# Kernel tuning notes

Hardware: AMD Instinct MI355X
Metric: run time of the kernel (lower is better)

The kernel has to match this reference:

```python
import jax, jax.numpy as jnp
import numpy as np
import math

B, L, D, H = 2, 2048, 1024, 16
DH = D // H  # d_head = 64
FACTOR = 5


def setup_inputs() -> dict:
    key = jax.random.key(0)
    ks = jax.random.split(key, 6)
    s = 0.02
    x = jax.random.normal(ks[0], (B, L, D), jnp.float32)
    Wq = jax.random.normal(ks[1], (D, D), jnp.float32) * s
    bq = jnp.zeros((D,), jnp.float32)
    Wkv = jax.random.normal(ks[2], (2 * D, D), jnp.float32) * s
    bkv = jnp.zeros((2 * D,), jnp.float32)
    Wout = jax.random.normal(ks[3], (D, D), jnp.float32) * s
    bout = jnp.zeros((D,), jnp.float32)
    U = min(FACTOR * math.ceil(math.log(L)), L)  # 40
    index_sample = jax.random.randint(ks[4], (L, U), 0, L, dtype=jnp.int32)
    return {"x": x, "Wq": Wq, "bq": bq, "Wkv": Wkv, "bkv": bkv,
            "Wout": Wout, "bout": bout, "index_sample": index_sample,
            "factor": FACTOR}


def reference(x, Wq, bq, Wkv, bkv, Wout, bout, index_sample, factor):
    b, l, d = x.shape
    h, dh = H, DH
    scale = 1.0 / math.sqrt(dh)
    u = min(factor * math.ceil(math.log(l)), l)

    # projections (torch Linear: y = x @ W.T + b)
    Q = (x @ Wq.T + bq).reshape(b, l, h, dh).transpose(0, 2, 1, 3)   # [B,H,L,dh]
    KV = x @ Wkv.T + bkv
    K, V = jnp.split(KV, 2, axis=-1)
    K = K.reshape(b, l, h, dh).transpose(0, 2, 1, 3)                  # [B,H,L,dh]
    V = V.reshape(b, l, h, dh).transpose(0, 2, 1, 3)                  # [B,H,L,dh]

    # sampled QK: per query position l, dot with U sampled keys
    K_s = K[:, :, index_sample, :]                                    # [B,H,L,U,dh]
    QK = jnp.einsum('bhld,bhlud->bhlu', Q, K_s)                       # [B,H,L,U]
    M = QK.max(axis=-1) - QK.mean(axis=-1)                            # sparsity measure
    _, top_idx = jax.lax.top_k(M, u)                                  # [B,H,u]

    # full attention only for the top-u queries
    top_q = jnp.take_along_axis(Q, top_idx[..., None], axis=2)        # [B,H,u,dh]
    scores = jnp.einsum('bhud,bhkd->bhuk', top_q, K) * scale          # [B,H,u,L]
    attn = jax.nn.softmax(scores, axis=-1)
    ctx_update = jnp.einsum('bhuk,bhkd->bhud', attn, V)               # [B,H,u,dh]

    # mean-initialized context, scatter updates at top queries
    context = jnp.broadcast_to(V.mean(axis=2, keepdims=True), (b, h, l, dh))
    bI = jnp.arange(b)[:, None, None]
    hI = jnp.arange(h)[None, :, None]
    context = context.at[bI, hI, top_idx].set(ctx_update)             # [B,H,L,dh]

    context = context.transpose(0, 2, 1, 3).reshape(b, l, d)
    return context @ Wout.T + bout
```

## Files before the change

### kernel.cpp

```cpp
#include <hip/hip_runtime.h>
#include <math.h>

#define B_ 2
#define L_ 2048
#define D_ 1024
#define H_ 16
#define DH_ 64
#define U_ 40
#define SCALE_ 0.125f

typedef __attribute__((ext_vector_type(8))) short short8v;
typedef __attribute__((ext_vector_type(4))) float f32x4;
typedef __attribute__((ext_vector_type(4))) unsigned short ushort4v;

static __device__ __forceinline__ unsigned short bf16_rne(float f) {
  unsigned int u = __float_as_uint(f);
  u += 0x7fff + ((u >> 16) & 1);
  return (unsigned short)(u >> 16);
}
static __device__ __forceinline__ float bf16_f32(unsigned short h) {
  return __uint_as_float(((unsigned int)h) << 16);
}

static __device__ __forceinline__ void gload16(const unsigned short* src,
                                               unsigned short* lds) {
  __builtin_amdgcn_global_load_lds(
      (const __attribute__((address_space(1))) void*)src,
      (__attribute__((address_space(3))) void*)lds, 16, 0, 0);
}

__global__ __launch_bounds__(256) void split_all(
    const float* __restrict__ Wq, const float* __restrict__ Wkv,
    const float* __restrict__ X, unsigned short* __restrict__ Whi,
    unsigned short* __restrict__ Wlo, unsigned short* __restrict__ Xhi,
    unsigned short* __restrict__ Xlo, float* __restrict__ vmAcc, int nW) {
  if (blockIdx.x == 0) {
    for (int z = threadIdx.x; z < B_ * D_; z += 256) vmAcc[z] = 0.f;
  }
  int i = blockIdx.x * 256 + threadIdx.x;
  const int nq_q = (D_ * D_) / 4;
  float4 v;
  unsigned short *hi, *lo;
  int off;
  if (i < nW) {
    v = (i < nq_q) ? ((const float4*)Wq)[i] : ((const float4*)Wkv)[i - nq_q];
    hi = Whi; lo = Wlo; off = i;
  } else {
    off = i - nW;
    v = ((const float4*)X)[off];
    hi = Xhi; lo = Xlo;
  }
  float vv[4] = {v.x, v.y, v.z, v.w};
  ushort4v h, l;
#pragma unroll
  for (int e = 0; e < 4; ++e) {
    unsigned short hh = bf16_rne(vv[e]);
    h[e] = hh;
    l[e] = bf16_rne(vv[e] - bf16_f32(hh));
  }
  ((ushort4v*)hi)[off] = h;
  ((ushort4v*)lo)[off] = l;
}

template <bool XS>
__global__ __launch_bounds__(256) void gemm_qkv_mfma(
    const float* __restrict__ X,
    const unsigned short* __restrict__ Xhi,
    const unsigned short* __restrict__ Xlo,
    const unsigned short* __restrict__ Whi,
    const unsigned short* __restrict__ Wlo,
    const float* __restrict__ bq, const float* __restrict__ bkv,
    float* __restrict__ Qo, float* __restrict__ Ko, float* __restrict__ Vo,
    float* __restrict__ vmAcc) {
  __shared__ unsigned short Ah[128 * 32];
  __shared__ unsigned short Al[128 * 32];
  __shared__ unsigned short Bh[128 * 32];
  __shared__ unsigned short Bl[128 * 32];
  const int tid = threadIdx.x;
  const int lane = tid & 63;
  const int wave = tid >> 6;
  const int wm = wave >> 1, wn = wave & 1;
  const int row0 = blockIdx.y * 128;
  const int col0 = blockIdx.x * 128;

  f32x4 acc[4][4] = {};

  const int grow = lane >> 2;
  const int gg = lane & 3;

  for (int k0 = 0; k0 < D_; k0 += 32) {
#pragma unroll
    for (int j = 0; j < 2; ++j) {
      int c = wave + 4 * j;
      int row = c * 16 + grow;
      int gsrc = (gg ^ ((row >> 1) & 3)) << 3;
      size_t soffB = (size_t)(col0 + row) * D_ + k0 + gsrc;
      gload16(Whi + soffB, Bh + c * 512);
      gload16(Wlo + soffB, Bl + c * 512);
      if (XS) {
        size_t soffA = (size_t)(row0 + row) * D_ + k0 + gsrc;
        gload16(Xhi + soffA, Ah + c * 512);
        gload16(Xlo + soffA, Al + c * 512);
      }
    }
    if (!XS) {
#pragma unroll
      for (int rep = 0; rep < 2; ++rep) {
        int task = tid + rep * 256;
        int row = task >> 2;
        int gt = task & 3;
        const float* s = X + (size_t)(row0 + row) * D_ + k0 + gt * 8;
        float4 a0 = *(const float4*)s;
        float4 a1 = *(const float4*)(s + 4);
        float av[8] = {a0.x, a0.y, a0.z, a0.w, a1.x, a1.y, a1.z, a1.w};
        short8v hseg, lseg;
#pragma unroll
        for (int e = 0; e < 8; ++e) {
          unsigned short hh = bf16_rne(av[e]);
          hseg[e] = (short)hh;
          lseg[e] = (short)bf16_rne(av[e] - bf16_f32(hh));
        }
        int dst = row * 32 + ((gt ^ ((row >> 1) & 3)) << 3);
        *(short8v*)&Ah[dst] = hseg;
        *(short8v*)&Al[dst] = lseg;
      }
    }
    __syncthreads();

    short8v a_h[4], a_l[4], b_h[4], b_l[4];
    const int hs = lane >> 4;
#pragma unroll
    for (int mi = 0; mi < 4; ++mi) {
      int rr = wm * 64 + mi * 16 + (lane & 15);
      int off = rr * 32 + ((hs ^ ((rr >> 1) & 3)) << 3);
      a_h[mi] = *(const short8v*)&Ah[off];
      a_l[mi] = *(const short8v*)&Al[off];
    }
#pragma unroll
    for (int ni = 0; ni < 4; ++ni) {
      int rc = wn * 64 + ni * 16 + (lane & 15);
      int off = rc * 32 + ((hs ^ ((rc >> 1) & 3)) << 3);
      b_h[ni] = *(const short8v*)&Bh[off];
      b_l[ni] = *(const short8v*)&Bl[off];
    }
#pragma unroll
    for (int mi = 0; mi < 4; ++mi)
#pragma unroll
      for (int ni = 0; ni < 4; ++ni) {
        acc[mi][ni] = __builtin_amdgcn_mfma_f32_16x16x32_bf16(
            a_h[mi], b_h[ni], acc[mi][ni], 0, 0, 0);
        acc[mi][ni] = __builtin_amdgcn_mfma_f32_16x16x32_bf16(
            a_h[mi], b_l[ni], acc[mi][ni], 0, 0, 0);
        acc[mi][ni] = __builtin_amdgcn_mfma_f32_16x16x32_bf16(
            a_l[mi], b_h[ni], acc[mi][ni], 0, 0, 0);
      }
    __syncthreads();
  }

#pragma unroll
  for (int ni = 0; ni < 4; ++ni) {
    int c = col0 + wn * 64 + ni * 16 + (lane & 15);
    int which = c >> 10;
    int jj = c & (D_ - 1);
    int h = jj >> 6, dh = jj & 63;
    float bias = (c < D_) ? bq[c] : bkv[c - D_];
    float* dst = (which == 0) ? Qo : ((which == 1) ? Ko : Vo);
#pragma unroll
    for (int mi = 0; mi < 4; ++mi) {
#pragma unroll
      for (int reg = 0; reg < 4; ++reg) {
        int r = row0 + wm * 64 + mi * 16 + ((lane >> 4) << 2) + reg;
        int b = r >> 11, l = r & (L_ - 1);
        dst[(((size_t)b * H_ + h) * L_ + l) * DH_ + dh] =
            acc[mi][ni][reg] + bias;
      }
    }
    if (which == 2) {
      float s = 0.f;
#pragma unroll
      for (int mi = 0; mi < 4; ++mi)
#pragma unroll
        for (int reg = 0; reg < 4; ++reg) s += acc[mi][ni][reg];
      s += __shfl_xor(s, 16);
      s += __shfl_xor(s, 32);
      if ((lane >> 4) == 0)
        atomicAdd(&vmAcc[(row0 >> 11) * D_ + jj], s + 64.0f * bias);
    }
  }
}

__global__ __launch_bounds__(256) void base_kernel(
    const float* __restrict__ vmAcc, const float* __restrict__ Wout,
    const float* __restrict__ bout, float* __restrict__ baseOut,
    float* __restrict__ vmeanM) {
  int bid = blockIdx.x;
  int b = bid >> 4, jc = bid & 15;
  int t = threadIdx.x;
  int j = jc * 64 + (t & 63);
  int isl = t >> 6;
  __shared__ float vm[D_];
  __shared__ float red[256];
  for (int i = t; i < D_; i += 256) vm[i] = vmAcc[b * D_ + i] * (1.0f / L_);
  __syncthreads();
  if (jc == 0)
    for (int i = t; i < D_; i += 256) vmeanM[b * D_ + i] = vm[i];
  float s = 0.f;
  const float* wr = Wout + (size_t)j * D_ + isl * 256;
  const float* vv = vm + isl * 256;
  for (int i = 0; i < 256; i += 4) {
    float4 w = *(const float4*)(wr + i);
    s += vv[i] * w.x + vv[i + 1] * w.y + vv[i + 2] * w.z + vv[i + 3] * w.w;
  }
  red[t] = s; __syncthreads();
  if (isl == 0)
    baseOut[b * D_ + j] =
        red[t] + red[t + 64] + red[t + 128] + red[t + 192] + bout[j];
}

__global__ __launch_bounds__(256) void bcast_out(
    const float* __restrict__ baseIn, float* __restrict__ out) {
  size_t i4 = (size_t)blockIdx.x * 256 + threadIdx.x;
  size_t i = i4 * 4;
  int b = (int)(i >> 21);
  int col = (int)(i & (D_ - 1));
  *(float4*)(out + i) = *(const float4*)(baseIn + b * D_ + col);
}

__global__ __launch_bounds__(256) void sample_m(
    const float* __restrict__ Q, const float* __restrict__ Kt,
    const int* __restrict__ idx, float* __restrict__ Mv) {
  int t = threadIdx.x;
  int w = t >> 6, lane = t & 63;
  int subl = lane >> 4, d16 = lane & 15;
  int gl = blockIdx.x * 16 + w * 4 + subl;
  int bh = gl >> 11, l = gl & (L_ - 1);
  const float4* Kb4 = (const float4*)(Kt + (size_t)bh * L_ * DH_);
  float4 q4 = ((const float4*)(Q + (size_t)gl * DH_))[d16];
  const int* irow = idx + l * U_;
  float mx = -INFINITY, sm = 0.f;
#pragma unroll 8
  for (int u = 0; u < U_; ++u) {
    int kl = irow[u];
    float4 k4 = Kb4[kl * 16 + d16];
    float p = q4.x * k4.x + q4.y * k4.y + q4.z * k4.z + q4.w * k4.w;
    p += __shfl_xor(p, 1);
    p += __shfl_xor(p, 2);
    p += __shfl_xor(p, 4);
    p += __shfl_xor(p, 8);
    mx = fmaxf(mx, p);
    sm += p;
  }
  if (d16 == 0) Mv[gl] = mx - sm * (1.0f / U_);
}

__global__ __launch_bounds__(64) void topk_kernel(
    const float* __restrict__ Mv, int* __restrict__ topIdx) {
  __shared__ float vals[L_];
  int lane = threadIdx.x;
  int bh = blockIdx.x;
  for (int j = 0; j < 32; ++j)
    vals[j * 64 + lane] = Mv[(size_t)bh * L_ + j * 64 + lane];
  __syncthreads();
  for (int it = 0; it < U_; ++it) {
    float bv = -INFINITY;
    int bi = 0x7fffffff;
    for (int j = 0; j < 32; ++j) {
      int i = j * 64 + lane;
      float v = vals[i];
      if (v > bv) { bv = v; bi = i; }
    }
#pragma unroll
    for (int off = 32; off > 0; off >>= 1) {
      float ov = __shfl_xor(bv, off);
      int oi = __shfl_xor(bi, off);
      if (ov > bv || (ov == bv && oi < bi)) { bv = ov; bi = oi; }
    }
    if (lane == 0) topIdx[bh * U_ + it] = bi;
    vals[bi] = -INFINITY;
    __syncthreads();
  }
}

__global__ __launch_bounds__(256) void attn_corr(
    const float* __restrict__ Q, const float* __restrict__ Kt,
    const float* __restrict__ Vt, const int* __restrict__ topIdx,
    const float* __restrict__ vmeanM, const float* __restrict__ Wout,
    float* __restrict__ out) {
  int qc = blockIdx.x;
  int bh = blockIdx.y;
  int b = bh >> 4, h = bh & (H_ - 1);
  __shared__ float Qs[5][DH_];
  __shared__ float Sv[5][L_];
  __shared__ float part[4][5][DH_];
  __shared__ float inv[5];
  __shared__ float dv[5][DH_];
  __shared__ int lq[5];
  int t = threadIdx.x;
  int lane = t & 63, w = t >> 6;

  if (t < 80) {
    int q = t >> 4, c4 = t & 15;
    int ql = topIdx[bh * U_ + qc * 5 + q];
    *(float4*)&Qs[q][c4 * 4] =
        *(const float4*)&Q[((size_t)bh * L_ + ql) * DH_ + c4 * 4];
  }
  if (t < 5) lq[t] = topIdx[bh * U_ + qc * 5 + t];
  __syncthreads();

  const float* Kb = Kt + (size_t)bh * L_ * DH_;
  for (int kc = 0; kc < 8; ++kc) {
    int key = kc * 256 + t;
    const float* kr = Kb + (size_t)key * DH_;
    float acc[5];
#pragma unroll
    for (int q = 0; q < 5; ++q) acc[q] = 0.f;
#pragma unroll
    for (int i4 = 0; i4 < 16; ++i4) {
      float4 k4 = *(const float4*)(kr + i4 * 4);
#pragma unroll
      for (int q = 0; q < 5; ++q) {
        float4 qv = *(const float4*)&Qs[q][i4 * 4];
        acc[q] += k4.x * qv.x + k4.y * qv.y + k4.z * qv.z + k4.w * qv.w;
      }
    }
#pragma unroll
    for (int q = 0; q < 5; ++q) Sv[q][key] = acc[q] * SCALE_;
  }
  __syncthreads();

#pragma unroll
  for (int rep = 0; rep < 2; ++rep) {
    int r = (rep == 0) ? w : (w == 0 ? 4 : -1);
    if (r >= 0) {
      float mx = -INFINITY;
      for (int j = 0; j < 32; ++j) mx = fmaxf(mx, Sv[r][j * 64 + lane]);
#pragma unroll
      for (int off = 1; off < 64; off <<= 1)
        mx = fmaxf(mx, __shfl_xor(mx, off));
      float sm = 0.f;
      for (int j = 0; j < 32; ++j) {
        float e = __expf(Sv[r][j * 64 + lane] - mx);
        Sv[r][j * 64 + lane] = e;
        sm += e;
      }
#pragma unroll
      for (int off = 1; off < 64; off <<= 1) sm += __shfl_xor(sm, off);
      if (lane == 0) inv[r] = 1.0f / sm;
    }
  }
  __syncthreads();

  {
    const float* vb = Vt + ((size_t)bh * L_ + w * 512) * DH_ + lane;
    float acc[5];
#pragma unroll
    for (int q = 0; q < 5; ++q) acc[q] = 0.f;
    for (int k4 = 0; k4 < 128; ++k4) {
      float v0 = vb[(k4 * 4 + 0) * DH_];
      float v1 = vb[(k4 * 4 + 1) * DH_];
      float v2 = vb[(k4 * 4 + 2) * DH_];
      float v3 = vb[(k4 * 4 + 3) * DH_];
      int k = w * 512 + k4 * 4;
#pragma unroll
      for (int q = 0; q < 5; ++q) {
        float4 p4 = *(const float4*)&Sv[q][k];
        acc[q] += p4.x * v0 + p4.y * v1 + p4.z * v2 + p4.w * v3;
      }
    }
#pragma unroll
    for (int q = 0; q < 5; ++q) part[w][q][lane] = acc[q];
  }
  __syncthreads();

  for (int o = t; o < 5 * DH_; o += 256) {
    int q = o >> 6, dh = o & 63;
    float s = (part[0][q][dh] + part[1][q][dh]) +
              (part[2][q][dh] + part[3][q][dh]);
    dv[q][dh] = s * inv[q] - vmeanM[b * D_ + h * DH_ + dh];
  }
  __syncthreads();

  int sub = t & 3;
  int jbase = t >> 2;
#pragma unroll
  for (int jc = 0; jc < 16; ++jc) {
    int j = jc * 64 + jbase;
    const float* wr = Wout + (size_t)j * D_ + h * DH_ + sub * 16;
    float4 w0 = ((const float4*)wr)[0];
    float4 w1 = ((const float4*)wr)[1];
    float4 w2 = ((const float4*)wr)[2];
    float4 w3 = ((const float4*)wr)[3];
#pragma unroll
    for (int q = 0; q < 5; ++q) {
      const float* dq = &dv[q][sub * 16];
      float s = dq[0] * w0.x + dq[1] * w0.y + dq[2] * w0.z + dq[3] * w0.w +
                dq[4] * w1.x + dq[5] * w1.y + dq[6] * w1.z + dq[7] * w1.w +
                dq[8] * w2.x + dq[9] * w2.y + dq[10] * w2.z + dq[11] * w2.w +
                dq[12] * w3.x + dq[13] * w3.y + dq[14] * w3.z + dq[15] * w3.w;
      s += __shfl_xor(s, 1);
      s += __shfl_xor(s, 2);
      if (sub == 0)
        atomicAdd(out + ((size_t)b * L_ + lq[q]) * D_ + j, s);
    }
  }
}

extern "C" void kernel_launch(void* const* d_in, const int* in_sizes, int n_in,
                              void* d_out, int out_size, void* d_ws,
                              size_t ws_size, hipStream_t stream) {
  const float* x    = (const float*)d_in[0];
  const float* Wq   = (const float*)d_in[1];
  const float* bq   = (const float*)d_in[2];
  const float* Wkv  = (const float*)d_in[3];
  const float* bkv  = (const float*)d_in[4];
  const float* Wout = (const float*)d_in[5];
  const float* bout = (const float*)d_in[6];
  const int*   idx  = (const int*)d_in[7];
  float* out = (float*)d_out;

  float* ws = (float*)d_ws;
  const size_t NQ = (size_t)B_ * H_ * L_ * DH_;
  float* Q  = ws;
  float* Kt = Q + NQ;
  float* Vt = Kt + NQ;
  unsigned short* Whi = (unsigned short*)(Vt + NQ);
  unsigned short* Wlo = Whi + (size_t)3 * D_ * D_;
  unsigned short* Xhi = Wlo + (size_t)3 * D_ * D_;
  unsigned short* Xlo = Xhi + NQ;
  float* Mv     = Vt + NQ;
  float* vmeanM = Mv + (size_t)B_ * H_ * L_;
  float* baseB  = vmeanM + B_ * D_;
  int*   topIdx = (int*)(baseB + B_ * D_);
  float* vmAcc = out;

  const bool xsplit = ws_size >= ((size_t)76 << 20);
  const int nW = 3 * D_ * D_ / 4;
  const int nX = (int)(NQ / 4);

  if (xsplit) {
    split_all<<<dim3((nW + nX) / 256), dim3(256), 0, stream>>>(
        Wq, Wkv, x, Whi, Wlo, Xhi, Xlo, vmAcc, nW);
    gemm_qkv_mfma<true>
        <<<dim3(3 * D_ / 128, B_ * L_ / 128), dim3(256), 0, stream>>>(
            x, Xhi, Xlo, Whi, Wlo, bq, bkv, Q, Kt, Vt, vmAcc);
  } else {
    split_all<<<dim3(nW / 256), dim3(256), 0, stream>>>(Wq, Wkv, x, Whi, Wlo,
                                                        Xhi, Xlo, vmAcc, nW);
    gemm_qkv_mfma<false>
        <<<dim3(3 * D_ / 128, B_ * L_ / 128), dim3(256), 0, stream>>>(
            x, Xhi, Xlo, Whi, Wlo, bq, bkv, Q, Kt, Vt, vmAcc);
  }
  base_kernel<<<dim3(B_ * 16), dim3(256), 0, stream>>>(vmAcc, Wout, bout,
                                                       baseB, vmeanM);
  bcast_out<<<dim3(B_ * L_ * D_ / 1024), dim3(256), 0, stream>>>(baseB, out);
  sample_m<<<dim3(B_ * H_ * L_ / 16), dim3(256), 0, stream>>>(Q, Kt, idx, Mv);
  topk_kernel<<<dim3(B_ * H_), dim3(64), 0, stream>>>(Mv, topIdx);
  attn_corr<<<dim3(8, 32), dim3(256), 0, stream>>>(Q, Kt, Vt, topIdx, vmeanM,
                                                   Wout, out);
}
```

Measured before the change: 259.6 us.

## Rewrite QKV GEMM as 8-wave triple-buffered pipelined kernel with 128x192 tiles

Replaces the 4-wave 128x128 QKV projection GEMM (split-bf16 emulation of fp32) with a 512-thread kernel using 128x192 tiles, a three-stage LDS ring buffer and phased interleaving of LDS reads, async global-to-LDS loads and MFMA bursts under raised wave priority. It aims to hide global-load latency and keep the matrix cores busy through explicit vmcnt/lgkmcnt waits and barriers. It costs more LDS per block and many barriers per k-step, and correctness depends on the hand-placed wait counts. The non-split fallback path is kept as a separate kernel.

Result: faster. 245.5 us (-5.4%).

```diff
diff --git a/kernel.cpp b/kernel.cpp
--- a/kernel.cpp
+++ b/kernel.cpp
@@ -28,6 +28,19 @@
       (const __attribute__((address_space(1))) void*)src,
       (__attribute__((address_space(3))) void*)lds, 16, 0, 0);
 }
+
+#define FENCE asm volatile("" ::: "memory")
+#define BARRIER                        \
+  do {                                 \
+    FENCE;                             \
+    __builtin_amdgcn_s_barrier();      \
+    FENCE;                             \
+  } while (0)
+#define LGKM0                                             \
+  do {                                                    \
+    asm volatile("s_waitcnt lgkmcnt(0)" ::: "memory");    \
+    __builtin_amdgcn_sched_barrier(0);                    \
+  } while (0)
 
 __global__ __launch_bounds__(256) void split_all(
     const float* __restrict__ Wq, const float* __restrict__ Wkv,
@@ -62,11 +75,156 @@
   ((ushort4v*)lo)[off] = l;
 }
 
-template <bool XS>
-__global__ __launch_bounds__(256) void gemm_qkv_mfma(
-    const float* __restrict__ X,
+__global__ __launch_bounds__(512, 2) void gemm_qkv_8ph(
     const unsigned short* __restrict__ Xhi,
     const unsigned short* __restrict__ Xlo,
+    const unsigned short* __restrict__ Whi,
+    const unsigned short* __restrict__ Wlo,
+    const float* __restrict__ bq, const float* __restrict__ bkv,
+    float* __restrict__ Qo, float* __restrict__ Ko, float* __restrict__ Vo,
+    float* __restrict__ vmAcc) {
+  __shared__ unsigned short LDS[3][20480];
+  const int tid = threadIdx.x;
+  const int lane = tid & 63;
+  const int wave = tid >> 6;
+  const int wm = wave >> 2, wn = wave & 3;
+  const int row0 = blockIdx.y * 128;
+  const int col0 = blockIdx.x * 192;
+
+  f32x4 acc[4][3] = {};
+
+  const unsigned short* gsrc[5];
+#pragma unroll
+  for (int r = 0; r < 5; ++r) {
+    int c = wave + 8 * r;
+    const unsigned short* base;
+    int rowin, isA;
+    if (c < 8)       { base = Xhi; rowin = c * 16;        isA = 1; }
+    else if (c < 16) { base = Xlo; rowin = (c - 8) * 16;  isA = 1; }
+    else if (c < 28) { base = Whi; rowin = (c - 16) * 16; isA = 0; }
+    else             { base = Wlo; rowin = (c - 28) * 16; isA = 0; }
+    rowin += (lane >> 2);
+    int grow = (isA ? row0 : col0) + rowin;
+    int seg = (lane & 3) ^ ((rowin >> 1) & 3);
+    gsrc[r] = base + (size_t)grow * D_ + seg * 8;
+  }
+
+  const int fr_r = lane & 15;
+  const int hs = lane >> 4;
+
+#define RD_A(mi)                                                     \
+  {                                                                  \
+    int rr = wm * 64 + (mi) * 16 + fr_r;                             \
+    int off = rr * 32 + ((hs ^ ((rr >> 1) & 3)) << 3);               \
+    a_h[mi] = *(const short8v*)&Lc[off];                             \
+    a_l[mi] = *(const short8v*)&Lc[4096 + off];                      \
+  }
+#define RD_B(ni)                                                     \
+  {                                                                  \
+    int rc = wn * 48 + (ni) * 16 + fr_r;                             \
+    int off = rc * 32 + ((hs ^ ((rc >> 1) & 3)) << 3);               \
+    b_h[ni] = *(const short8v*)&Lc[8192 + off];                      \
+    b_l[ni] = *(const short8v*)&Lc[14336 + off];                     \
+  }
+#define MM3(mi, ni)                                                  \
+  acc[mi][ni] = __builtin_amdgcn_mfma_f32_16x16x32_bf16(             \
+      a_h[mi], b_h[ni], acc[mi][ni], 0, 0, 0);                       \
+  acc[mi][ni] = __builtin_amdgcn_mfma_f32_16x16x32_bf16(             \
+      a_h[mi], b_l[ni], acc[mi][ni], 0, 0, 0);                       \
+  acc[mi][ni] = __builtin_amdgcn_mfma_f32_16x16x32_bf16(             \
+      a_l[mi], b_h[ni], acc[mi][ni], 0, 0, 0);
+#define STG(r, k0s, Ls) \
+  gload16(gsrc[r] + (k0s), (Ls) + (wave + 8 * (r)) * 512)
+
+  {
+    unsigned short* L0 = &LDS[0][0];
+    unsigned short* L1 = &LDS[1][0];
+    STG(0, 0, L0); STG(1, 0, L0); STG(2, 0, L0); STG(3, 0, L0); STG(4, 0, L0);
+    STG(0, 32, L1); STG(1, 32, L1); STG(2, 32, L1); STG(3, 32, L1);
+    STG(4, 32, L1);
+  }
+  asm volatile("s_waitcnt vmcnt(5)" ::: "memory");
+  BARRIER;
+
+  for (int ks = 0; ks < 32; ++ks) {
+    int cur = ks % 3;
+    int stg = (ks + 2) % 3;
+    int k0s = (ks + 2) * 32;
+    unsigned short* Lc = &LDS[cur][0];
+    unsigned short* Ls = &LDS[stg][0];
+    short8v a_h[4], a_l[4], b_h[3], b_l[3];
+
+    RD_A(0) RD_A(1) RD_B(0)
+    if (ks < 30) { STG(0, k0s, Ls); STG(1, k0s, Ls); }
+    BARRIER;
+    LGKM0;
+    __builtin_amdgcn_s_setprio(1);
+    MM3(0, 0) MM3(1, 0)
+    __builtin_amdgcn_s_setprio(0);
+    BARRIER;
+
+    RD_A(2) RD_B(1)
+    if (ks < 30) { STG(2, k0s, Ls); STG(3, k0s, Ls); }
+    BARRIER;
+    LGKM0;
+    __builtin_amdgcn_s_setprio(1);
+    MM3(2, 0) MM3(0, 1) MM3(1, 1) MM3(2, 1)
+    __builtin_amdgcn_s_setprio(0);
+    BARRIER;
+
+    RD_A(3) RD_B(2)
+    if (ks < 30) { STG(4, k0s, Ls); }
+    BARRIER;
+    LGKM0;
+    __builtin_amdgcn_s_setprio(1);
+    MM3(3, 0) MM3(3, 1) MM3(0, 2) MM3(1, 2) MM3(2, 2) MM3(3, 2)
+    __builtin_amdgcn_s_setprio(0);
+    if (ks < 30) {
+      asm volatile("s_waitcnt vmcnt(5)" ::: "memory");
+    } else {
+      asm volatile("s_waitcnt vmcnt(0)" ::: "memory");
+    }
+    BARRIER;
+  }
+
+#pragma unroll
+  for (int ni = 0; ni < 3; ++ni) {
+    int c = col0 + wn * 48 + ni * 16 + (lane & 15);
+    int which = c >> 10;
+    int jj = c & (D_ - 1);
+    int h = jj >> 6, dh = jj & 63;
+    float bias = (c < D_) ? bq[c] : bkv[c - D_];
+    float* dst = (which == 0) ? Qo : ((which == 1) ? Ko : Vo);
+#pragma unroll
+    for (int mi = 0; mi < 4; ++mi) {
+#pragma unroll
+      for (int reg = 0; reg < 4; ++reg) {
+        int r = row0 + wm * 64 + mi * 16 + ((lane >> 4) << 2) + reg;
+        int b = r >> 11, l = r & (L_ - 1);
+        dst[(((size_t)b * H_ + h) * L_ + l) * DH_ + dh] =
+            acc[mi][ni][reg] + bias;
+      }
+    }
+    if (which == 2) {
+      float s = 0.f;
+#pragma unroll
+      for (int mi = 0; mi < 4; ++mi)
+#pragma unroll
+        for (int reg = 0; reg < 4; ++reg) s += acc[mi][ni][reg];
+      s += __shfl_xor(s, 16);
+      s += __shfl_xor(s, 32);
+      if ((lane >> 4) == 0)
+        atomicAdd(&vmAcc[(row0 >> 11) * D_ + jj], s + 64.0f * bias);
+    }
+  }
+#undef RD_A
+#undef RD_B
+#undef MM3
+#undef STG
+}
+
+__global__ __launch_bounds__(256) void gemm_qkv_fallback(
+    const float* __restrict__ X,
     const unsigned short* __restrict__ Whi,
     const unsigned short* __restrict__ Wlo,
     const float* __restrict__ bq, const float* __restrict__ bkv,
@@ -97,33 +255,26 @@
       size_t soffB = (size_t)(col0 + row) * D_ + k0 + gsrc;
       gload16(Whi + soffB, Bh + c * 512);
       gload16(Wlo + soffB, Bl + c * 512);
-      if (XS) {
-        size_t soffA = (size_t)(row0 + row) * D_ + k0 + gsrc;
-        gload16(Xhi + soffA, Ah + c * 512);
-        gload16(Xlo + soffA, Al + c * 512);
+    }
+#pragma unroll
+    for (int rep = 0; rep < 2; ++rep) {
+      int task = tid + rep * 256;
+      int row = task >> 2;
+      int gt = task & 3;
+      const float* s = X + (size_t)(row0 + row) * D_ + k0 + gt * 8;
+      float4 a0 = *(const float4*)s;
+      float4 a1 = *(const float4*)(s + 4);
+      float av[8] = {a0.x, a0.y, a0.z, a0.w, a1.x, a1.y, a1.z, a1.w};
+      short8v hseg, lseg;
+#pragma unroll
+      for (int e = 0; e < 8; ++e) {
+        unsigned short hh = bf16_rne(av[e]);
+        hseg[e] = (short)hh;
+        lseg[e] = (short)bf16_rne(av[e] - bf16_f32(hh));
       }
-    }
-    if (!XS) {
-#pragma unroll
-      for (int rep = 0; rep < 2; ++rep) {
-        int task = tid + rep * 256;
-        int row = task >> 2;
-        int gt = task & 3;
-        const float* s = X + (size_t)(row0 + row) * D_ + k0 + gt * 8;
-        float4 a0 = *(const float4*)s;
-        float4 a1 = *(const float4*)(s + 4);
-        float av[8] = {a0.x, a0.y, a0.z, a0.w, a1.x, a1.y, a1.z, a1.w};
-        short8v hseg, lseg;
-#pragma unroll
-        for (int e = 0; e < 8; ++e) {
-          unsigned short hh = bf16_rne(av[e]);
-          hseg[e] = (short)hh;
-          lseg[e] = (short)bf16_rne(av[e] - bf16_f32(hh));
-        }
-        int dst = row * 32 + ((gt ^ ((row >> 1) & 3)) << 3);
-        *(short8v*)&Ah[dst] = hseg;
-        *(short8v*)&Al[dst] = lseg;
-      }
+      int dst = row * 32 + ((gt ^ ((row >> 1) & 3)) << 3);
+      *(short8v*)&Ah[dst] = hseg;
+      *(short8v*)&Al[dst] = lseg;
     }
     __syncthreads();
 
@@ -440,15 +591,13 @@
   if (xsplit) {
     split_all<<<dim3((nW + nX) / 256), dim3(256), 0, stream>>>(
         Wq, Wkv, x, Whi, Wlo, Xhi, Xlo, vmAcc, nW);
-    gemm_qkv_mfma<true>
-        <<<dim3(3 * D_ / 128, B_ * L_ / 128), dim3(256), 0, stream>>>(
-            x, Xhi, Xlo, Whi, Wlo, bq, bkv, Q, Kt, Vt, vmAcc);
+    gemm_qkv_8ph<<<dim3(3 * D_ / 192, B_ * L_ / 128), dim3(512), 0, stream>>>(
+        Xhi, Xlo, Whi, Wlo, bq, bkv, Q, Kt, Vt, vmAcc);
   } else {
     split_all<<<dim3(nW / 256), dim3(256), 0, stream>>>(Wq, Wkv, x, Whi, Wlo,
                                                         Xhi, Xlo, vmAcc, nW);
-    gemm_qkv_mfma<false>
-        <<<dim3(3 * D_ / 128, B_ * L_ / 128), dim3(256), 0, stream>>>(
-            x, Xhi, Xlo, Whi, Wlo, bq, bkv, Q, Kt, Vt, vmAcc);
+    gemm_qkv_fallback<<<dim3(3 * D_ / 128, B_ * L_ / 128), dim3(256), 0,
+                        stream>>>(x, Whi, Wlo, bq, bkv, Q, Kt, Vt, vmAcc);
   }
   base_kernel<<<dim3(B_ * 16), dim3(256), 0, stream>>>(vmAcc, Wout, bout,
                                                        baseB, vmeanM);
```
